# Optimization experiments

Hardware: AMD Instinct MI355X
Metric: run time of the kernel (lower is better)

The kernel has to match this reference:

```python
import jax, jax.numpy as jnp
import numpy as np

T, BS, N = 256, 512, 2048
FUDGE = 1e-4


def setup_inputs() -> dict:
    key = jax.random.key(0)
    ks = jax.random.split(key, 6)
    f32 = jnp.float32
    return {
        "noises": jax.random.normal(ks[0], (T, BS), f32) * 0.1,  # per-step process noise [T, bs]
        "ys": jax.random.normal(ks[1], (T,), f32),               # per-step scalar targets
        "qs": jax.random.normal(ks[2], (T,), f32),               # per-step scalar context input
        "z_biases": jax.random.normal(ks[3], (N,), f32),         # random-feature bias directions
        "w_in": jax.random.normal(ks[4], (N,), f32),             # random input weights
        "w_inq": jax.random.normal(ks[5], (N,), f32),            # random q-input weights
        # scalar learned params (legacy init values)
        "log_learning_rate": jnp.array(-6.0, f32),
        "log_learning_rate_decay": jnp.array(0.0, f32),
        "sigma_b": jnp.array(0.1, f32),
        "output_scale": jnp.array(1.0, f32),
        "u_feedback_scale": jnp.array(1.0, f32),
        "log_weight_decay": jnp.array(-0.001, f32),
        "q_scale": jnp.array(1.0, f32),
        "tauqlpf_m1": jnp.array(-1.0, f32),
        "tauylpf_m1": jnp.array(-1.0, f32),
    }


def _forward(noises, ys, qs, z_biases, w_in, w_inq,
             log_learning_rate, log_learning_rate_decay, sigma_b,
             output_scale, u_feedback_scale, log_weight_decay, q_scale,
             tauqlpf_m1, tauylpf_m1):
    bs = noises.shape[1]
    n = w_in.shape[0]
    softplus = lambda v: jnp.log1p(jnp.exp(v))
    biases = sigma_b * z_biases                    # [n]
    lr0 = jnp.exp(log_learning_rate)               # scalar
    tauq = 1.0 + softplus(tauqlpf_m1)
    tauy = 1.0 + softplus(tauylpf_m1)
    wd = jnp.exp(log_weight_decay)                 # tie_lr_weight_decay=False -> scalar decay
    lr_decay_rate = jnp.exp(log_learning_rate_decay)

    def step(carry, inp):
        w_out, u, e, lr_mult, qlp, ylp = carry
        y, noise_x, q = inp
        qlp = (1.0 - tauq) * qlp + tauq * q
        q_in = w_inq * (q_scale * qlp)             # [n]
        x = u * u_feedback_scale + e + noise_x     # noise injected at node 'x'; [bs]
        h = jax.nn.relu(biases[None, :] + x[:, None] * w_in[None, :] + q_in[None, :])  # [bs, n]
        u = jnp.einsum('kj,kj->k', w_out, h)       # [bs]
        a_mean = output_scale * u                  # [bs]
        # y observed every step (no None/NaN branch)
        ylp = (1.0 - tauy) * ylp + tauy * y
        e = ylp - u                                # [bs]
        lr = lr0 * lr_mult                         # [bs]
        dw = e[:, None] * h * lr[:, None]          # [bs, n]
        w_out = w_out + dw
        norms = jnp.sqrt(FUDGE + jnp.sum(dw * dw, axis=1))
        lr_mult = lr_mult * jnp.exp(-lr_decay_rate * norms)
        w_out = wd * w_out
        return (w_out, u, e, lr_mult, qlp, ylp), a_mean

    init = (jnp.zeros((bs, n), noises.dtype),
            jnp.zeros((bs,), noises.dtype),
            jnp.zeros((bs,), noises.dtype),
            jnp.ones((bs,), noises.dtype),
            jnp.zeros((), noises.dtype),
            jnp.zeros((), noises.dtype))
    _, a_means = jax.lax.scan(step, init, (ys, noises, qs))
    return a_means  # [T, bs]


def reference(noises, ys, qs, z_biases, w_in, w_inq,
              log_learning_rate, log_learning_rate_decay, sigma_b,
              output_scale, u_feedback_scale, log_weight_decay, q_scale,
              tauqlpf_m1, tauylpf_m1):
    return _forward(noises, ys, qs, z_biases, w_in, w_inq,
                    log_learning_rate, log_learning_rate_decay, sigma_b,
                    output_scale, u_feedback_scale, log_weight_decay, q_scale,
                    tauqlpf_m1, tauylpf_m1)
```

## Files before the change

kernel.cpp:

```cpp
#include <hip/hip_runtime.h>
#include <math.h>
#include <stdint.h>

#define T_STEPS 256
#define BS      512
#define N       2048
#define BLOCK   64
#define FUDGE   1e-4f

__global__ __launch_bounds__(BLOCK) __attribute__((amdgpu_waves_per_eu(1, 1)))
void legacy_elbo_scan_kernel(
    const float* __restrict__ noises,
    const float* __restrict__ ys,
    const float* __restrict__ qs,
    const float* __restrict__ z_biases,
    const float* __restrict__ w_in,
    const float* __restrict__ w_inq,
    const float* __restrict__ p_llr,
    const float* __restrict__ p_llrd,
    const float* __restrict__ p_sigb,
    const float* __restrict__ p_oscale,
    const float* __restrict__ p_ufs,
    const float* __restrict__ p_lwd,
    const float* __restrict__ p_qscale,
    const float* __restrict__ p_tauq,
    const float* __restrict__ p_tauy,
    float* __restrict__ out)
{
    const int tid = threadIdx.x;
    const int blk = blockIdx.x;

    const float sigb    = p_sigb[0];
    const float lr0     = expf(p_llr[0]);
    const float lr_decay= expf(p_llrd[0]);
    const float wd      = expf(p_lwd[0]);
    const float rwd     = 1.0f / wd;
    const float tauq    = 1.0f + log1pf(expf(p_tauq[0]));
    const float tauy    = 1.0f + log1pf(expf(p_tauy[0]));
    const float omtq    = 1.0f - tauq;
    const float omty    = 1.0f - tauy;
    const float qscale  = p_qscale[0];
    const float ufs     = p_ufs[0];
    const float oscale  = p_oscale[0];
    const float nld2    = -lr_decay * 1.4426950408889634f;

    const float* nzp = noises + blk;
    const int    ovo = blk * 4;

    asm volatile(
        "v_lshlrev_b32 v7, 4, %[vtid]\n\t"
        "v_add_u32 v5, 0x1000, v7\n\t"
        "global_load_dwordx4 v[32:35],  v7, %[pzb]\n\t"
        "global_load_dwordx4 v[36:39],  v7, %[pzb] offset:1024\n\t"
        "global_load_dwordx4 v[40:43],  v7, %[pzb] offset:2048\n\t"
        "global_load_dwordx4 v[44:47],  v7, %[pzb] offset:3072\n\t"
        "global_load_dwordx4 v[48:51],  v5, %[pzb]\n\t"
        "global_load_dwordx4 v[52:55],  v5, %[pzb] offset:1024\n\t"
        "global_load_dwordx4 v[56:59],  v5, %[pzb] offset:2048\n\t"
        "global_load_dwordx4 v[60:63],  v5, %[pzb] offset:3072\n\t"
        "global_load_dwordx4 v[64:67],  v7, %[pwi]\n\t"
        "global_load_dwordx4 v[68:71],  v7, %[pwi] offset:1024\n\t"
        "global_load_dwordx4 v[72:75],  v7, %[pwi] offset:2048\n\t"
        "global_load_dwordx4 v[76:79],  v7, %[pwi] offset:3072\n\t"
        "global_load_dwordx4 v[80:83],  v5, %[pwi]\n\t"
        "global_load_dwordx4 v[84:87],  v5, %[pwi] offset:1024\n\t"
        "global_load_dwordx4 v[88:91],  v5, %[pwi] offset:2048\n\t"
        "global_load_dwordx4 v[92:95],  v5, %[pwi] offset:3072\n\t"
        "global_load_dwordx4 v[96:99],  v7, %[pwq]\n\t"
        "global_load_dwordx4 v[100:103], v7, %[pwq] offset:1024\n\t"
        "global_load_dwordx4 v[104:107], v7, %[pwq] offset:2048\n\t"
        "global_load_dwordx4 v[108:111], v7, %[pwq] offset:3072\n\t"
        "global_load_dwordx4 v[112:115], v5, %[pwq]\n\t"
        "global_load_dwordx4 v[116:119], v5, %[pwq] offset:1024\n\t"
        "global_load_dwordx4 v[120:123], v5, %[pwq] offset:2048\n\t"
        "global_load_dwordx4 v[124:127], v5, %[pwq] offset:3072\n\t"
        "s_waitcnt vmcnt(0)\n\t"
        "v_mul_f32 v32, %[osg], v32\n\t"  "v_mul_f32 v33, %[osg], v33\n\t"
        "v_mul_f32 v34, %[osg], v34\n\t"  "v_mul_f32 v35, %[osg], v35\n\t"
        "v_mul_f32 v36, %[osg], v36\n\t"  "v_mul_f32 v37, %[osg], v37\n\t"
        "v_mul_f32 v38, %[osg], v38\n\t"  "v_mul_f32 v39, %[osg], v39\n\t"
        "v_mul_f32 v40, %[osg], v40\n\t"  "v_mul_f32 v41, %[osg], v41\n\t"
        "v_mul_f32 v42, %[osg], v42\n\t"  "v_mul_f32 v43, %[osg], v43\n\t"
        "v_mul_f32 v44, %[osg], v44\n\t"  "v_mul_f32 v45, %[osg], v45\n\t"
        "v_mul_f32 v46, %[osg], v46\n\t"  "v_mul_f32 v47, %[osg], v47\n\t"
        "v_mul_f32 v48, %[osg], v48\n\t"  "v_mul_f32 v49, %[osg], v49\n\t"
        "v_mul_f32 v50, %[osg], v50\n\t"  "v_mul_f32 v51, %[osg], v51\n\t"
        "v_mul_f32 v52, %[osg], v52\n\t"  "v_mul_f32 v53, %[osg], v53\n\t"
        "v_mul_f32 v54, %[osg], v54\n\t"  "v_mul_f32 v55, %[osg], v55\n\t"
        "v_mul_f32 v56, %[osg], v56\n\t"  "v_mul_f32 v57, %[osg], v57\n\t"
        "v_mul_f32 v58, %[osg], v58\n\t"  "v_mul_f32 v59, %[osg], v59\n\t"
        "v_mul_f32 v60, %[osg], v60\n\t"  "v_mul_f32 v61, %[osg], v61\n\t"
        "v_mul_f32 v62, %[osg], v62\n\t"  "v_mul_f32 v63, %[osg], v63\n\t"
        "v_mov_b32 v128, 0\n\t" "v_mov_b32 v129, 0\n\t" "v_mov_b32 v130, 0\n\t" "v_mov_b32 v131, 0\n\t"
        "v_mov_b32 v132, 0\n\t" "v_mov_b32 v133, 0\n\t" "v_mov_b32 v134, 0\n\t" "v_mov_b32 v135, 0\n\t"
        "v_mov_b32 v136, 0\n\t" "v_mov_b32 v137, 0\n\t" "v_mov_b32 v138, 0\n\t" "v_mov_b32 v139, 0\n\t"
        "v_mov_b32 v140, 0\n\t" "v_mov_b32 v141, 0\n\t" "v_mov_b32 v142, 0\n\t" "v_mov_b32 v143, 0\n\t"
        "v_mov_b32 v144, 0\n\t" "v_mov_b32 v145, 0\n\t" "v_mov_b32 v146, 0\n\t" "v_mov_b32 v147, 0\n\t"
        "v_mov_b32 v148, 0\n\t" "v_mov_b32 v149, 0\n\t" "v_mov_b32 v150, 0\n\t" "v_mov_b32 v151, 0\n\t"
        "v_mov_b32 v152, 0\n\t" "v_mov_b32 v153, 0\n\t" "v_mov_b32 v154, 0\n\t" "v_mov_b32 v155, 0\n\t"
        "v_mov_b32 v156, 0\n\t" "v_mov_b32 v157, 0\n\t" "v_mov_b32 v158, 0\n\t" "v_mov_b32 v159, 0\n\t"
        "v_mov_b32 v20, 0\n\t" "v_mov_b32 v21, 0\n\t" "v_mov_b32 v22, 0\n\t" "v_mov_b32 v23, 0\n\t"
        "v_mov_b32 v24, 1.0\n\t" "v_mov_b32 v25, 1.0\n\t" "v_mov_b32 v26, 1.0\n\t"
        "v_mov_b32 v6, %[ovo]\n\t"
        "s_mov_b32 s60, 0\n\t"
        "s_mov_b32 s61, 0\n\t"
        "s_mov_b32 s62, 0\n\t"
        "s_load_dword s66, %[pys], s61\n\t"
        "s_load_dword s67, %[pqs], s61\n\t"
        "s_load_dword s68, %[pnz], s62\n\t"
        "s_waitcnt lgkmcnt(0)\n\t"
        "Lelbo0:\n\t"
        "s_add_u32 s63, s61, 4\n\t"
        "s_min_u32 s63, s63, 0x3fc\n\t"
        "s_add_u32 s64, s62, 0x800\n\t"
        "s_min_u32 s64, s64, 0x7f800\n\t"
        "s_load_dword s69, %[pys], s63\n\t"
        "s_load_dword s70, %[pqs], s63\n\t"
        "s_load_dword s71, %[pnz], s64\n\t"
        "v_mov_b32 v30, s67\n\t"
        "v_mul_f32 v20, %[omq], v20\n\t"
        "v_fmac_f32 v20, %[otq], v30\n\t"
        "v_mul_f32 v10, %[oq], v20\n\t"
        "v_mov_b32 v11, v10\n\t"
        "v_mov_b32 v8, s68\n\t"
        "v_add_f32 v8, v23, v8\n\t"
        "v_fmac_f32 v8, %[ouf], v22\n\t"
        "v_mov_b32 v9, v8\n\t"
        "v_mov_b32 v12, 0\n\t" "v_mov_b32 v13, 0\n\t" "v_mov_b32 v14, 0\n\t" "v_mov_b32 v15, 0\n\t"
        "v_mov_b32 v16, 0\n\t" "v_mov_b32 v17, 0\n\t" "v_mov_b32 v18, 0\n\t" "v_mov_b32 v19, 0\n\t"
        "v_pk_fma_f32 v[160:161], v[10:11], v[96:97],  v[32:33]\n\t"
        "v_pk_fma_f32 v[162:163], v[10:11], v[98:99],  v[34:35]\n\t"
        "v_pk_fma_f32 v[164:165], v[10:11], v[100:101], v[36:37]\n\t"
        "v_pk_fma_f32 v[166:167], v[10:11], v[102:103], v[38:39]\n\t"
        "v_pk_fma_f32 v[168:169], v[10:11], v[104:105], v[40:41]\n\t"
        "v_pk_fma_f32 v[170:171], v[10:11], v[106:107], v[42:43]\n\t"
        "v_pk_fma_f32 v[172:173], v[10:11], v[108:109], v[44:45]\n\t"
        "v_pk_fma_f32 v[174:175], v[10:11], v[110:111], v[46:47]\n\t"
        "v_pk_fma_f32 v[176:177], v[10:11], v[112:113], v[48:49]\n\t"
        "v_pk_fma_f32 v[178:179], v[10:11], v[114:115], v[50:51]\n\t"
        "v_pk_fma_f32 v[180:181], v[10:11], v[116:117], v[52:53]\n\t"
        "v_pk_fma_f32 v[182:183], v[10:11], v[118:119], v[54:55]\n\t"
        "v_pk_fma_f32 v[184:185], v[10:11], v[120:121], v[56:57]\n\t"
        "v_pk_fma_f32 v[186:187], v[10:11], v[122:123], v[58:59]\n\t"
        "v_pk_fma_f32 v[188:189], v[10:11], v[124:125], v[60:61]\n\t"
        "v_pk_fma_f32 v[190:191], v[10:11], v[126:127], v[62:63]\n\t"
        "v_pk_fma_f32 v[160:161], v[8:9], v[64:65], v[160:161]\n\t"
        "v_pk_fma_f32 v[162:163], v[8:9], v[66:67], v[162:163]\n\t"
        "v_pk_fma_f32 v[164:165], v[8:9], v[68:69], v[164:165]\n\t"
        "v_pk_fma_f32 v[166:167], v[8:9], v[70:71], v[166:167]\n\t"
        "v_pk_fma_f32 v[168:169], v[8:9], v[72:73], v[168:169]\n\t"
        "v_pk_fma_f32 v[170:171], v[8:9], v[74:75], v[170:171]\n\t"
        "v_pk_fma_f32 v[172:173], v[8:9], v[76:77], v[172:173]\n\t"
        "v_pk_fma_f32 v[174:175], v[8:9], v[78:79], v[174:175]\n\t"
        "v_pk_fma_f32 v[176:177], v[8:9], v[80:81], v[176:177]\n\t"
        "v_pk_fma_f32 v[178:179], v[8:9], v[82:83], v[178:179]\n\t"
        "v_pk_fma_f32 v[180:181], v[8:9], v[84:85], v[180:181]\n\t"
        "v_pk_fma_f32 v[182:183], v[8:9], v[86:87], v[182:183]\n\t"
        "v_pk_fma_f32 v[184:185], v[8:9], v[88:89], v[184:185]\n\t"
        "v_pk_fma_f32 v[186:187], v[8:9], v[90:91], v[186:187]\n\t"
        "v_pk_fma_f32 v[188:189], v[8:9], v[92:93], v[188:189]\n\t"
        "v_pk_fma_f32 v[190:191], v[8:9], v[94:95], v[190:191]\n\t"
        "v_max_f32 v160, 0, v160\n\t" "v_max_f32 v161, 0, v161\n\t"
        "v_max_f32 v162, 0, v162\n\t" "v_max_f32 v163, 0, v163\n\t"
        "v_max_f32 v164, 0, v164\n\t" "v_max_f32 v165, 0, v165\n\t"
        "v_max_f32 v166, 0, v166\n\t" "v_max_f32 v167, 0, v167\n\t"
        "v_max_f32 v168, 0, v168\n\t" "v_max_f32 v169, 0, v169\n\t"
        "v_max_f32 v170, 0, v170\n\t" "v_max_f32 v171, 0, v171\n\t"
        "v_max_f32 v172, 0, v172\n\t" "v_max_f32 v173, 0, v173\n\t"
        "v_max_f32 v174, 0, v174\n\t" "v_max_f32 v175, 0, v175\n\t"
        "v_max_f32 v176, 0, v176\n\t" "v_max_f32 v177, 0, v177\n\t"
        "v_max_f32 v178, 0, v178\n\t" "v_max_f32 v179, 0, v179\n\t"
        "v_max_f32 v180, 0, v180\n\t" "v_max_f32 v181, 0, v181\n\t"
        "v_max_f32 v182, 0, v182\n\t" "v_max_f32 v183, 0, v183\n\t"
        "v_max_f32 v184, 0, v184\n\t" "v_max_f32 v185, 0, v185\n\t"
        "v_max_f32 v186, 0, v186\n\t" "v_max_f32 v187, 0, v187\n\t"
        "v_max_f32 v188, 0, v188\n\t" "v_max_f32 v189, 0, v189\n\t"
        "v_max_f32 v190, 0, v190\n\t" "v_max_f32 v191, 0, v191\n\t"
        "v_pk_fma_f32 v[12:13], v[128:129], v[160:161], v[12:13]\n\t"
        "v_pk_fma_f32 v[16:17], v[160:161], v[160:161], v[16:17]\n\t"
        "v_pk_fma_f32 v[14:15], v[130:131], v[162:163], v[14:15]\n\t"
        "v_pk_fma_f32 v[18:19], v[162:163], v[162:163], v[18:19]\n\t"
        "v_pk_fma_f32 v[12:13], v[132:133], v[164:165], v[12:13]\n\t"
        "v_pk_fma_f32 v[16:17], v[164:165], v[164:165], v[16:17]\n\t"
        "v_pk_fma_f32 v[14:15], v[134:135], v[166:167], v[14:15]\n\t"
        "v_pk_fma_f32 v[18:19], v[166:167], v[166:167], v[18:19]\n\t"
        "v_pk_fma_f32 v[12:13], v[136:137], v[168:169], v[12:13]\n\t"
        "v_pk_fma_f32 v[16:17], v[168:169], v[168:169], v[16:17]\n\t"
        "v_pk_fma_f32 v[14:15], v[138:139], v[170:171], v[14:15]\n\t"
        "v_pk_fma_f32 v[18:19], v[170:171], v[170:171], v[18:19]\n\t"
        "v_pk_fma_f32 v[12:13], v[140:141], v[172:173], v[12:13]\n\t"
        "v_pk_fma_f32 v[16:17], v[172:173], v[172:173], v[16:17]\n\t"
        "v_pk_fma_f32 v[14:15], v[142:143], v[174:175], v[14:15]\n\t"
        "v_pk_fma_f32 v[18:19], v[174:175], v[174:175], v[18:19]\n\t"
        "v_pk_fma_f32 v[12:13], v[144:145], v[176:177], v[12:13]\n\t"
        "v_pk_fma_f32 v[16:17], v[176:177], v[176:177], v[16:17]\n\t"
        "v_pk_fma_f32 v[14:15], v[146:147], v[178:179], v[14:15]\n\t"
        "v_pk_fma_f32 v[18:19], v[178:179], v[178:179], v[18:19]\n\t"
        "v_pk_fma_f32 v[12:13], v[148:149], v[180:181], v[12:13]\n\t"
        "v_pk_fma_f32 v[16:17], v[180:181], v[180:181], v[16:17]\n\t"
        "v_pk_fma_f32 v[14:15], v[150:151], v[182:183], v[14:15]\n\t"
        "v_pk_fma_f32 v[18:19], v[182:183], v[182:183], v[18:19]\n\t"
        "v_pk_fma_f32 v[12:13], v[152:153], v[184:185], v[12:13]\n\t"
        "v_pk_fma_f32 v[16:17], v[184:185], v[184:185], v[16:17]\n\t"
        "v_pk_fma_f32 v[14:15], v[154:155], v[186:187], v[14:15]\n\t"
        "v_pk_fma_f32 v[18:19], v[186:187], v[186:187], v[18:19]\n\t"
        "v_pk_fma_f32 v[12:13], v[156:157], v[188:189], v[12:13]\n\t"
        "v_pk_fma_f32 v[16:17], v[188:189], v[188:189], v[16:17]\n\t"
        "v_pk_fma_f32 v[14:15], v[158:159], v[190:191], v[14:15]\n\t"
        "v_pk_fma_f32 v[18:19], v[190:191], v[190:191], v[18:19]\n\t"
        "v_add_f32 v12, v12, v14\n\t"
        "v_add_f32 v13, v13, v15\n\t"
        "v_add_f32 v16, v16, v18\n\t"
        "v_add_f32 v17, v17, v19\n\t"
        "v_add_f32 v12, v12, v13\n\t"
        "v_add_f32 v16, v16, v17\n\t"
        "s_nop 1\n\t"
        "v_mov_b32_dpp v30, v12 row_shr:1 row_mask:0xf bank_mask:0xf\n\t"
        "v_mov_b32_dpp v31, v16 row_shr:1 row_mask:0xf bank_mask:0xf\n\t"
        "v_add_f32 v12, v12, v30\n\t"
        "v_add_f32 v16, v16, v31\n\t"
        "s_nop 0\n\t"
        "v_mov_b32_dpp v30, v12 row_shr:2 row_mask:0xf bank_mask:0xf\n\t"
        "v_mov_b32_dpp v31, v16 row_shr:2 row_mask:0xf bank_mask:0xf\n\t"
        "v_add_f32 v12, v12, v30\n\t"
        "v_add_f32 v16, v16, v31\n\t"
        "s_nop 0\n\t"
        "v_mov_b32_dpp v30, v12 row_shr:4 row_mask:0xf bank_mask:0xf\n\t"
        "v_mov_b32_dpp v31, v16 row_shr:4 row_mask:0xf bank_mask:0xf\n\t"
        "v_add_f32 v12, v12, v30\n\t"
        "v_add_f32 v16, v16, v31\n\t"
        "s_nop 0\n\t"
        "v_mov_b32_dpp v30, v12 row_shr:8 row_mask:0xf bank_mask:0xf\n\t"
        "v_mov_b32_dpp v31, v16 row_shr:8 row_mask:0xf bank_mask:0xf\n\t"
        "v_add_f32 v12, v12, v30\n\t"
        "v_add_f32 v16, v16, v31\n\t"
        "s_nop 0\n\t"
        "v_mov_b32_dpp v30, v12 row_bcast:15 row_mask:0xf bank_mask:0xf\n\t"
        "v_mov_b32_dpp v31, v16 row_bcast:15 row_mask:0xf bank_mask:0xf\n\t"
        "v_add_f32 v12, v12, v30\n\t"
        "v_add_f32 v16, v16, v31\n\t"
        "s_nop 0\n\t"
        "v_mov_b32_dpp v30, v12 row_bcast:31 row_mask:0xf bank_mask:0xf\n\t"
        "v_mov_b32_dpp v31, v16 row_bcast:31 row_mask:0xf bank_mask:0xf\n\t"
        "v_add_f32 v12, v12, v30\n\t"
        "v_add_f32 v16, v16, v31\n\t"
        "s_nop 1\n\t"
        "v_readlane_b32 s74, v12, 63\n\t"
        "v_readlane_b32 s75, v16, 63\n\t"
        "v_mul_f32 v22, s74, v25\n\t"
        "v_mul_f32 v30, %[oos], v22\n\t"
        "s_mov_b64 s[72:73], exec\n\t"
        "s_mov_b64 exec, 1\n\t"
        "global_store_dword v6, v30, %[pou]\n\t"
        "s_mov_b64 exec, s[72:73]\n\t"
        "v_add_u32 v6, 0x800, v6\n\t"
        "v_mov_b32 v30, s66\n\t"
        "v_mul_f32 v21, %[omy], v21\n\t"
        "v_fmac_f32 v21, %[oty], v30\n\t"
        "v_sub_f32 v23, v21, v22\n\t"
        "v_mul_f32 v27, %[olr], v23\n\t"
        "v_mul_f32 v27, v27, v24\n\t"
        "v_mul_f32 v28, v27, v26\n\t"
        "v_mov_b32 v29, v28\n\t"
        "v_pk_fma_f32 v[128:129], v[28:29], v[160:161], v[128:129]\n\t"
        "v_pk_fma_f32 v[130:131], v[28:29], v[162:163], v[130:131]\n\t"
        "v_pk_fma_f32 v[132:133], v[28:29], v[164:165], v[132:133]\n\t"
        "v_pk_fma_f32 v[134:135], v[28:29], v[166:167], v[134:135]\n\t"
        "v_pk_fma_f32 v[136:137], v[28:29], v[168:169], v[136:137]\n\t"
        "v_pk_fma_f32 v[138:139], v[28:29], v[170:171], v[138:139]\n\t"
        "v_pk_fma_f32 v[140:141], v[28:29], v[172:173], v[140:141]\n\t"
        "v_pk_fma_f32 v[142:143], v[28:29], v[174:175], v[142:143]\n\t"
        "v_pk_fma_f32 v[144:145], v[28:29], v[176:177], v[144:145]\n\t"
        "v_pk_fma_f32 v[146:147], v[28:29], v[178:179], v[146:147]\n\t"
        "v_pk_fma_f32 v[148:149], v[28:29], v[180:181], v[148:149]\n\t"
        "v_pk_fma_f32 v[150:151], v[28:29], v[182:183], v[150:151]\n\t"
        "v_pk_fma_f32 v[152:153], v[28:29], v[184:185], v[152:153]\n\t"
        "v_pk_fma_f32 v[154:155], v[28:29], v[186:187], v[154:155]\n\t"
        "v_pk_fma_f32 v[156:157], v[28:29], v[188:189], v[156:157]\n\t"
        "v_pk_fma_f32 v[158:159], v[28:29], v[190:191], v[158:159]\n\t"
        "v_mul_f32 v30, v27, v27\n\t"
        "v_mul_f32 v30, s75, v30\n\t"
        "v_add_f32 v30, 0x38d1b717, v30\n\t"
        "v_sqrt_f32 v30, v30\n\t"
        "s_nop 1\n\t"
        "v_mul_f32 v30, %[ond], v30\n\t"
        "v_exp_f32 v30, v30\n\t"
        "s_nop 1\n\t"
        "v_mul_f32 v24, v24, v30\n\t"
        "v_mul_f32 v25, %[owd], v25\n\t"
        "v_mul_f32 v26, %[orw], v26\n\t"
        "s_waitcnt lgkmcnt(0)\n\t"
        "s_mov_b32 s66, s69\n\t"
        "s_mov_b32 s67, s70\n\t"
        "s_mov_b32 s68, s71\n\t"
        "s_mov_b32 s61, s63\n\t"
        "s_mov_b32 s62, s64\n\t"
        "s_add_u32 s60, s60, 1\n\t"
        "s_cmp_lt_u32 s60, 0x100\n\t"
        "s_cbranch_scc1 Lelbo0\n\t"
        "s_waitcnt vmcnt(0)\n\t"
        :
        : [pys]"s"(ys), [pqs]"s"(qs), [pnz]"s"(nzp), [pou]"s"(out),
          [pzb]"s"(z_biases), [pwi]"s"(w_in), [pwq]"s"(w_inq),
          [vtid]"v"(tid), [ovo]"v"(ovo),
          [osg]"v"(sigb), [otq]"v"(tauq), [omq]"v"(omtq),
          [oty]"v"(tauy), [omy]"v"(omty), [oq]"v"(qscale),
          [ouf]"v"(ufs), [olr]"v"(lr0), [owd]"v"(wd), [orw]"v"(rwd),
          [oos]"v"(oscale), [ond]"v"(nld2)
        : "memory", "scc",
          "s60","s61","s62","s63","s64","s65","s66","s67","s68","s69",
          "s70","s71","s72","s73","s74","s75",
          "v2","v3","v4","v5","v6","v7","v8","v9","v10","v11",
          "v12","v13","v14","v15","v16","v17","v18","v19","v20","v21",
          "v22","v23","v24","v25","v26","v27","v28","v29","v30","v31",
          "v32","v33","v34","v35","v36","v37","v38","v39","v40","v41",
          "v42","v43","v44","v45","v46","v47","v48","v49","v50","v51",
          "v52","v53","v54","v55","v56","v57","v58","v59","v60","v61",
          "v62","v63","v64","v65","v66","v67","v68","v69","v70","v71",
          "v72","v73","v74","v75","v76","v77","v78","v79","v80","v81",
          "v82","v83","v84","v85","v86","v87","v88","v89","v90","v91",
          "v92","v93","v94","v95","v96","v97","v98","v99","v100","v101",
          "v102","v103","v104","v105","v106","v107","v108","v109","v110","v111",
          "v112","v113","v114","v115","v116","v117","v118","v119","v120","v121",
          "v122","v123","v124","v125","v126","v127","v128","v129","v130","v131",
          "v132","v133","v134","v135","v136","v137","v138","v139","v140","v141",
          "v142","v143","v144","v145","v146","v147","v148","v149","v150","v151",
          "v152","v153","v154","v155","v156","v157","v158","v159","v160","v161",
          "v162","v163","v164","v165","v166","v167","v168","v169","v170","v171",
          "v172","v173","v174","v175","v176","v177","v178","v179","v180","v181",
          "v182","v183","v184","v185","v186","v187","v188","v189","v190","v191"
    );
}

extern "C" void kernel_launch(void* const* d_in, const int* in_sizes, int n_in,
                              void* d_out, int out_size, void* d_ws, size_t ws_size,
                              hipStream_t stream) {
    (void)in_sizes; (void)n_in; (void)d_ws; (void)ws_size; (void)out_size;
    const float* noises   = (const float*)d_in[0];
    const float* ys       = (const float*)d_in[1];
    const float* qs       = (const float*)d_in[2];
    const float* z_biases = (const float*)d_in[3];
    const float* w_in     = (const float*)d_in[4];
    const float* w_inq    = (const float*)d_in[5];
    const float* llr      = (const float*)d_in[6];
    const float* llrd     = (const float*)d_in[7];
    const float* sigb     = (const float*)d_in[8];
    const float* oscale   = (const float*)d_in[9];
    const float* ufs      = (const float*)d_in[10];
    const float* lwd      = (const float*)d_in[11];
    const float* qscale   = (const float*)d_in[12];
    const float* tauq     = (const float*)d_in[13];
    const float* tauy     = (const float*)d_in[14];
    float* out = (float*)d_out;

    hipLaunchKernelGGL(legacy_elbo_scan_kernel, dim3(BS), dim3(BLOCK), 0, stream,
                       noises, ys, qs, z_biases, w_in, w_inq,
                       llr, llrd, sigb, oscale, ufs, lwd, qscale, tauq, tauy,
                       out);
}
```

Baseline: 199.4 us.

## Split feature dimension across four waves with LDS cross-wave reduction

Each block grows from one wave to four, and each thread now owns 8 of the 2048 features instead of 32. Register use drops sharply and a block can occupy all SIMDs of a CU. The per-step dot product and squared-norm sums are first reduced within each wave using DPP. The four wave partials are then combined through a double-buffered LDS slot with a barrier every step. This shortens the serial per-step instruction chain, at the cost of a workgroup barrier and an LDS round trip on each of the 256 dependent steps.

```diff
diff --git a/kernel.cpp b/kernel.cpp
--- a/kernel.cpp
+++ b/kernel.cpp
@@ -5,10 +5,10 @@
 #define T_STEPS 256
 #define BS      512
 #define N       2048
-#define BLOCK   64
+#define BLOCK   256
 #define FUDGE   1e-4f
 
-__global__ __launch_bounds__(BLOCK) __attribute__((amdgpu_waves_per_eu(1, 1)))
+__global__ __launch_bounds__(BLOCK, 2)
 void legacy_elbo_scan_kernel(
     const float* __restrict__ noises,
     const float* __restrict__ ys,
@@ -30,6 +30,10 @@
     const int tid = threadIdx.x;
     const int blk = blockIdx.x;
 
+    __shared__ float red_lds[16];
+    if (tid < 16) red_lds[tid] = 0.0f;
+    __syncthreads();
+
     const float sigb    = p_sigb[0];
     const float lr0     = expf(p_llr[0]);
     const float lr_decay= expf(p_llrd[0]);
@@ -48,57 +52,29 @@
     const int    ovo = blk * 4;
 
     asm volatile(
-        "v_lshlrev_b32 v7, 4, %[vtid]\n\t"
-        "v_add_u32 v5, 0x1000, v7\n\t"
-        "global_load_dwordx4 v[32:35],  v7, %[pzb]\n\t"
-        "global_load_dwordx4 v[36:39],  v7, %[pzb] offset:1024\n\t"
-        "global_load_dwordx4 v[40:43],  v7, %[pzb] offset:2048\n\t"
-        "global_load_dwordx4 v[44:47],  v7, %[pzb] offset:3072\n\t"
-        "global_load_dwordx4 v[48:51],  v5, %[pzb]\n\t"
-        "global_load_dwordx4 v[52:55],  v5, %[pzb] offset:1024\n\t"
-        "global_load_dwordx4 v[56:59],  v5, %[pzb] offset:2048\n\t"
-        "global_load_dwordx4 v[60:63],  v5, %[pzb] offset:3072\n\t"
-        "global_load_dwordx4 v[64:67],  v7, %[pwi]\n\t"
-        "global_load_dwordx4 v[68:71],  v7, %[pwi] offset:1024\n\t"
-        "global_load_dwordx4 v[72:75],  v7, %[pwi] offset:2048\n\t"
-        "global_load_dwordx4 v[76:79],  v7, %[pwi] offset:3072\n\t"
-        "global_load_dwordx4 v[80:83],  v5, %[pwi]\n\t"
-        "global_load_dwordx4 v[84:87],  v5, %[pwi] offset:1024\n\t"
-        "global_load_dwordx4 v[88:91],  v5, %[pwi] offset:2048\n\t"
-        "global_load_dwordx4 v[92:95],  v5, %[pwi] offset:3072\n\t"
-        "global_load_dwordx4 v[96:99],  v7, %[pwq]\n\t"
-        "global_load_dwordx4 v[100:103], v7, %[pwq] offset:1024\n\t"
-        "global_load_dwordx4 v[104:107], v7, %[pwq] offset:2048\n\t"
-        "global_load_dwordx4 v[108:111], v7, %[pwq] offset:3072\n\t"
-        "global_load_dwordx4 v[112:115], v5, %[pwq]\n\t"
-        "global_load_dwordx4 v[116:119], v5, %[pwq] offset:1024\n\t"
-        "global_load_dwordx4 v[120:123], v5, %[pwq] offset:2048\n\t"
-        "global_load_dwordx4 v[124:127], v5, %[pwq] offset:3072\n\t"
+        "v_lshrrev_b32 v3, 6, %[vtid]\n\t"
+        "v_lshlrev_b32 v4, 3, v3\n\t"
+        "v_and_b32 v7, 63, %[vtid]\n\t"
+        "v_cmp_eq_u32 vcc, 63, v7\n\t"
+        "s_mov_b64 s[74:75], vcc\n\t"
+        "v_cmp_eq_u32 vcc, 0, %[vtid]\n\t"
+        "s_mov_b64 s[76:77], vcc\n\t"
+        "v_mov_b32 v5, 0\n\t"
+        "v_lshlrev_b32 v1, 4, %[vtid]\n\t"
+        "v_add_u32 v2, 0x1000, v1\n\t"
+        "global_load_dwordx4 v[40:43], v1, %[pzb]\n\t"
+        "global_load_dwordx4 v[44:47], v2, %[pzb]\n\t"
+        "global_load_dwordx4 v[48:51], v1, %[pwi]\n\t"
+        "global_load_dwordx4 v[52:55], v2, %[pwi]\n\t"
+        "global_load_dwordx4 v[56:59], v1, %[pwq]\n\t"
+        "global_load_dwordx4 v[60:63], v2, %[pwq]\n\t"
         "s_waitcnt vmcnt(0)\n\t"
-        "v_mul_f32 v32, %[osg], v32\n\t"  "v_mul_f32 v33, %[osg], v33\n\t"
-        "v_mul_f32 v34, %[osg], v34\n\t"  "v_mul_f32 v35, %[osg], v35\n\t"
-        "v_mul_f32 v36, %[osg], v36\n\t"  "v_mul_f32 v37, %[osg], v37\n\t"
-        "v_mul_f32 v38, %[osg], v38\n\t"  "v_mul_f32 v39, %[osg], v39\n\t"
         "v_mul_f32 v40, %[osg], v40\n\t"  "v_mul_f32 v41, %[osg], v41\n\t"
         "v_mul_f32 v42, %[osg], v42\n\t"  "v_mul_f32 v43, %[osg], v43\n\t"
         "v_mul_f32 v44, %[osg], v44\n\t"  "v_mul_f32 v45, %[osg], v45\n\t"
         "v_mul_f32 v46, %[osg], v46\n\t"  "v_mul_f32 v47, %[osg], v47\n\t"
-        "v_mul_f32 v48, %[osg], v48\n\t"  "v_mul_f32 v49, %[osg], v49\n\t"
-        "v_mul_f32 v50, %[osg], v50\n\t"  "v_mul_f32 v51, %[osg], v51\n\t"
-        "v_mul_f32 v52, %[osg], v52\n\t"  "v_mul_f32 v53, %[osg], v53\n\t"
-        "v_mul_f32 v54, %[osg], v54\n\t"  "v_mul_f32 v55, %[osg], v55\n\t"
-        "v_mul_f32 v56, %[osg], v56\n\t"  "v_mul_f32 v57, %[osg], v57\n\t"
-        "v_mul_f32 v58, %[osg], v58\n\t"  "v_mul_f32 v59, %[osg], v59\n\t"
-        "v_mul_f32 v60, %[osg], v60\n\t"  "v_mul_f32 v61, %[osg], v61\n\t"
-        "v_mul_f32 v62, %[osg], v62\n\t"  "v_mul_f32 v63, %[osg], v63\n\t"
-        "v_mov_b32 v128, 0\n\t" "v_mov_b32 v129, 0\n\t" "v_mov_b32 v130, 0\n\t" "v_mov_b32 v131, 0\n\t"
-        "v_mov_b32 v132, 0\n\t" "v_mov_b32 v133, 0\n\t" "v_mov_b32 v134, 0\n\t" "v_mov_b32 v135, 0\n\t"
-        "v_mov_b32 v136, 0\n\t" "v_mov_b32 v137, 0\n\t" "v_mov_b32 v138, 0\n\t" "v_mov_b32 v139, 0\n\t"
-        "v_mov_b32 v140, 0\n\t" "v_mov_b32 v141, 0\n\t" "v_mov_b32 v142, 0\n\t" "v_mov_b32 v143, 0\n\t"
-        "v_mov_b32 v144, 0\n\t" "v_mov_b32 v145, 0\n\t" "v_mov_b32 v146, 0\n\t" "v_mov_b32 v147, 0\n\t"
-        "v_mov_b32 v148, 0\n\t" "v_mov_b32 v149, 0\n\t" "v_mov_b32 v150, 0\n\t" "v_mov_b32 v151, 0\n\t"
-        "v_mov_b32 v152, 0\n\t" "v_mov_b32 v153, 0\n\t" "v_mov_b32 v154, 0\n\t" "v_mov_b32 v155, 0\n\t"
-        "v_mov_b32 v156, 0\n\t" "v_mov_b32 v157, 0\n\t" "v_mov_b32 v158, 0\n\t" "v_mov_b32 v159, 0\n\t"
+        "v_mov_b32 v64, 0\n\t" "v_mov_b32 v65, 0\n\t" "v_mov_b32 v66, 0\n\t" "v_mov_b32 v67, 0\n\t"
+        "v_mov_b32 v68, 0\n\t" "v_mov_b32 v69, 0\n\t" "v_mov_b32 v70, 0\n\t" "v_mov_b32 v71, 0\n\t"
         "v_mov_b32 v20, 0\n\t" "v_mov_b32 v21, 0\n\t" "v_mov_b32 v22, 0\n\t" "v_mov_b32 v23, 0\n\t"
         "v_mov_b32 v24, 1.0\n\t" "v_mov_b32 v25, 1.0\n\t" "v_mov_b32 v26, 1.0\n\t"
         "v_mov_b32 v6, %[ovo]\n\t"
@@ -109,7 +85,7 @@
         "s_load_dword s67, %[pqs], s61\n\t"
         "s_load_dword s68, %[pnz], s62\n\t"
         "s_waitcnt lgkmcnt(0)\n\t"
-        "Lelbo0:\n\t"
+        "Lelbo2:\n\t"
         "s_add_u32 s63, s61, 4\n\t"
         "s_min_u32 s63, s63, 0x3fc\n\t"
         "s_add_u32 s64, s62, 0x800\n\t"
@@ -126,131 +102,75 @@
         "v_add_f32 v8, v23, v8\n\t"
         "v_fmac_f32 v8, %[ouf], v22\n\t"
         "v_mov_b32 v9, v8\n\t"
-        "v_mov_b32 v12, 0\n\t" "v_mov_b32 v13, 0\n\t" "v_mov_b32 v14, 0\n\t" "v_mov_b32 v15, 0\n\t"
-        "v_mov_b32 v16, 0\n\t" "v_mov_b32 v17, 0\n\t" "v_mov_b32 v18, 0\n\t" "v_mov_b32 v19, 0\n\t"
-        "v_pk_fma_f32 v[160:161], v[10:11], v[96:97],  v[32:33]\n\t"
-        "v_pk_fma_f32 v[162:163], v[10:11], v[98:99],  v[34:35]\n\t"
-        "v_pk_fma_f32 v[164:165], v[10:11], v[100:101], v[36:37]\n\t"
-        "v_pk_fma_f32 v[166:167], v[10:11], v[102:103], v[38:39]\n\t"
-        "v_pk_fma_f32 v[168:169], v[10:11], v[104:105], v[40:41]\n\t"
-        "v_pk_fma_f32 v[170:171], v[10:11], v[106:107], v[42:43]\n\t"
-        "v_pk_fma_f32 v[172:173], v[10:11], v[108:109], v[44:45]\n\t"
-        "v_pk_fma_f32 v[174:175], v[10:11], v[110:111], v[46:47]\n\t"
-        "v_pk_fma_f32 v[176:177], v[10:11], v[112:113], v[48:49]\n\t"
-        "v_pk_fma_f32 v[178:179], v[10:11], v[114:115], v[50:51]\n\t"
-        "v_pk_fma_f32 v[180:181], v[10:11], v[116:117], v[52:53]\n\t"
-        "v_pk_fma_f32 v[182:183], v[10:11], v[118:119], v[54:55]\n\t"
-        "v_pk_fma_f32 v[184:185], v[10:11], v[120:121], v[56:57]\n\t"
-        "v_pk_fma_f32 v[186:187], v[10:11], v[122:123], v[58:59]\n\t"
-        "v_pk_fma_f32 v[188:189], v[10:11], v[124:125], v[60:61]\n\t"
-        "v_pk_fma_f32 v[190:191], v[10:11], v[126:127], v[62:63]\n\t"
-        "v_pk_fma_f32 v[160:161], v[8:9], v[64:65], v[160:161]\n\t"
-        "v_pk_fma_f32 v[162:163], v[8:9], v[66:67], v[162:163]\n\t"
-        "v_pk_fma_f32 v[164:165], v[8:9], v[68:69], v[164:165]\n\t"
-        "v_pk_fma_f32 v[166:167], v[8:9], v[70:71], v[166:167]\n\t"
-        "v_pk_fma_f32 v[168:169], v[8:9], v[72:73], v[168:169]\n\t"
-        "v_pk_fma_f32 v[170:171], v[8:9], v[74:75], v[170:171]\n\t"
-        "v_pk_fma_f32 v[172:173], v[8:9], v[76:77], v[172:173]\n\t"
-        "v_pk_fma_f32 v[174:175], v[8:9], v[78:79], v[174:175]\n\t"
-        "v_pk_fma_f32 v[176:177], v[8:9], v[80:81], v[176:177]\n\t"
-        "v_pk_fma_f32 v[178:179], v[8:9], v[82:83], v[178:179]\n\t"
-        "v_pk_fma_f32 v[180:181], v[8:9], v[84:85], v[180:181]\n\t"
-        "v_pk_fma_f32 v[182:183], v[8:9], v[86:87], v[182:183]\n\t"
-        "v_pk_fma_f32 v[184:185], v[8:9], v[88:89], v[184:185]\n\t"
-        "v_pk_fma_f32 v[186:187], v[8:9], v[90:91], v[186:187]\n\t"
-        "v_pk_fma_f32 v[188:189], v[8:9], v[92:93], v[188:189]\n\t"
-        "v_pk_fma_f32 v[190:191], v[8:9], v[94:95], v[190:191]\n\t"
-        "v_max_f32 v160, 0, v160\n\t" "v_max_f32 v161, 0, v161\n\t"
-        "v_max_f32 v162, 0, v162\n\t" "v_max_f32 v163, 0, v163\n\t"
-        "v_max_f32 v164, 0, v164\n\t" "v_max_f32 v165, 0, v165\n\t"
-        "v_max_f32 v166, 0, v166\n\t" "v_max_f32 v167, 0, v167\n\t"
-        "v_max_f32 v168, 0, v168\n\t" "v_max_f32 v169, 0, v169\n\t"
-        "v_max_f32 v170, 0, v170\n\t" "v_max_f32 v171, 0, v171\n\t"
-        "v_max_f32 v172, 0, v172\n\t" "v_max_f32 v173, 0, v173\n\t"
-        "v_max_f32 v174, 0, v174\n\t" "v_max_f32 v175, 0, v175\n\t"
-        "v_max_f32 v176, 0, v176\n\t" "v_max_f32 v177, 0, v177\n\t"
-        "v_max_f32 v178, 0, v178\n\t" "v_max_f32 v179, 0, v179\n\t"
-        "v_max_f32 v180, 0, v180\n\t" "v_max_f32 v181, 0, v181\n\t"
-        "v_max_f32 v182, 0, v182\n\t" "v_max_f32 v183, 0, v183\n\t"
-        "v_max_f32 v184, 0, v184\n\t" "v_max_f32 v185, 0, v185\n\t"
-        "v_max_f32 v186, 0, v186\n\t" "v_max_f32 v187, 0, v187\n\t"
-        "v_max_f32 v188, 0, v188\n\t" "v_max_f32 v189, 0, v189\n\t"
-        "v_max_f32 v190, 0, v190\n\t" "v_max_f32 v191, 0, v191\n\t"
-        "v_pk_fma_f32 v[12:13], v[128:129], v[160:161], v[12:13]\n\t"
-        "v_pk_fma_f32 v[16:17], v[160:161], v[160:161], v[16:17]\n\t"
-        "v_pk_fma_f32 v[14:15], v[130:131], v[162:163], v[14:15]\n\t"
-        "v_pk_fma_f32 v[18:19], v[162:163], v[162:163], v[18:19]\n\t"
-        "v_pk_fma_f32 v[12:13], v[132:133], v[164:165], v[12:13]\n\t"
-        "v_pk_fma_f32 v[16:17], v[164:165], v[164:165], v[16:17]\n\t"
-        "v_pk_fma_f32 v[14:15], v[134:135], v[166:167], v[14:15]\n\t"
-        "v_pk_fma_f32 v[18:19], v[166:167], v[166:167], v[18:19]\n\t"
-        "v_pk_fma_f32 v[12:13], v[136:137], v[168:169], v[12:13]\n\t"
-        "v_pk_fma_f32 v[16:17], v[168:169], v[168:169], v[16:17]\n\t"
-        "v_pk_fma_f32 v[14:15], v[138:139], v[170:171], v[14:15]\n\t"
-        "v_pk_fma_f32 v[18:19], v[170:171], v[170:171], v[18:19]\n\t"
-        "v_pk_fma_f32 v[12:13], v[140:141], v[172:173], v[12:13]\n\t"
-        "v_pk_fma_f32 v[16:17], v[172:173], v[172:173], v[16:17]\n\t"
-        "v_pk_fma_f32 v[14:15], v[142:143], v[174:175], v[14:15]\n\t"
-        "v_pk_fma_f32 v[18:19], v[174:175], v[174:175], v[18:19]\n\t"
-        "v_pk_fma_f32 v[12:13], v[144:145], v[176:177], v[12:13]\n\t"
-        "v_pk_fma_f32 v[16:17], v[176:177], v[176:177], v[16:17]\n\t"
-        "v_pk_fma_f32 v[14:15], v[146:147], v[178:179], v[14:15]\n\t"
-        "v_pk_fma_f32 v[18:19], v[178:179], v[178:179], v[18:19]\n\t"
-        "v_pk_fma_f32 v[12:13], v[148:149], v[180:181], v[12:13]\n\t"
-        "v_pk_fma_f32 v[16:17], v[180:181], v[180:181], v[16:17]\n\t"
-        "v_pk_fma_f32 v[14:15], v[150:151], v[182:183], v[14:15]\n\t"
-        "v_pk_fma_f32 v[18:19], v[182:183], v[182:183], v[18:19]\n\t"
-        "v_pk_fma_f32 v[12:13], v[152:153], v[184:185], v[12:13]\n\t"
-        "v_pk_fma_f32 v[16:17], v[184:185], v[184:185], v[16:17]\n\t"
-        "v_pk_fma_f32 v[14:15], v[154:155], v[186:187], v[14:15]\n\t"
-        "v_pk_fma_f32 v[18:19], v[186:187], v[186:187], v[18:19]\n\t"
-        "v_pk_fma_f32 v[12:13], v[156:157], v[188:189], v[12:13]\n\t"
-        "v_pk_fma_f32 v[16:17], v[188:189], v[188:189], v[16:17]\n\t"
-        "v_pk_fma_f32 v[14:15], v[158:159], v[190:191], v[14:15]\n\t"
-        "v_pk_fma_f32 v[18:19], v[190:191], v[190:191], v[18:19]\n\t"
-        "v_add_f32 v12, v12, v14\n\t"
-        "v_add_f32 v13, v13, v15\n\t"
-        "v_add_f32 v16, v16, v18\n\t"
-        "v_add_f32 v17, v17, v19\n\t"
+        "v_mov_b32 v12, 0\n\t" "v_mov_b32 v13, 0\n\t"
+        "v_mov_b32 v14, 0\n\t" "v_mov_b32 v15, 0\n\t"
+        "v_pk_fma_f32 v[72:73], v[10:11], v[56:57], v[40:41]\n\t"
+        "v_pk_fma_f32 v[74:75], v[10:11], v[58:59], v[42:43]\n\t"
+        "v_pk_fma_f32 v[76:77], v[10:11], v[60:61], v[44:45]\n\t"
+        "v_pk_fma_f32 v[78:79], v[10:11], v[62:63], v[46:47]\n\t"
+        "v_pk_fma_f32 v[72:73], v[8:9], v[48:49], v[72:73]\n\t"
+        "v_pk_fma_f32 v[74:75], v[8:9], v[50:51], v[74:75]\n\t"
+        "v_pk_fma_f32 v[76:77], v[8:9], v[52:53], v[76:77]\n\t"
+        "v_pk_fma_f32 v[78:79], v[8:9], v[54:55], v[78:79]\n\t"
+        "v_max_f32 v72, 0, v72\n\t" "v_max_f32 v73, 0, v73\n\t"
+        "v_max_f32 v74, 0, v74\n\t" "v_max_f32 v75, 0, v75\n\t"
+        "v_max_f32 v76, 0, v76\n\t" "v_max_f32 v77, 0, v77\n\t"
+        "v_max_f32 v78, 0, v78\n\t" "v_max_f32 v79, 0, v79\n\t"
+        "v_pk_fma_f32 v[12:13], v[64:65], v[72:73], v[12:13]\n\t"
+        "v_pk_fma_f32 v[14:15], v[72:73], v[72:73], v[14:15]\n\t"
+        "v_pk_fma_f32 v[12:13], v[66:67], v[74:75], v[12:13]\n\t"
+        "v_pk_fma_f32 v[14:15], v[74:75], v[74:75], v[14:15]\n\t"
+        "v_pk_fma_f32 v[12:13], v[68:69], v[76:77], v[12:13]\n\t"
+        "v_pk_fma_f32 v[14:15], v[76:77], v[76:77], v[14:15]\n\t"
+        "v_pk_fma_f32 v[12:13], v[70:71], v[78:79], v[12:13]\n\t"
+        "v_pk_fma_f32 v[14:15], v[78:79], v[78:79], v[14:15]\n\t"
         "v_add_f32 v12, v12, v13\n\t"
-        "v_add_f32 v16, v16, v17\n\t"
+        "v_add_f32 v14, v14, v15\n\t"
         "s_nop 1\n\t"
         "v_mov_b32_dpp v30, v12 row_shr:1 row_mask:0xf bank_mask:0xf\n\t"
-        "v_mov_b32_dpp v31, v16 row_shr:1 row_mask:0xf bank_mask:0xf\n\t"
-        "v_add_f32 v12, v12, v30\n\t"
-        "v_add_f32 v16, v16, v31\n\t"
+        "v_mov_b32_dpp v31, v14 row_shr:1 row_mask:0xf bank_mask:0xf\n\t"
+        "v_add_f32 v12, v12, v30\n\t"
+        "v_add_f32 v14, v14, v31\n\t"
         "s_nop 0\n\t"
         "v_mov_b32_dpp v30, v12 row_shr:2 row_mask:0xf bank_mask:0xf\n\t"
-        "v_mov_b32_dpp v31, v16 row_shr:2 row_mask:0xf bank_mask:0xf\n\t"
-        "v_add_f32 v12, v12, v30\n\t"
-        "v_add_f32 v16, v16, v31\n\t"
+        "v_mov_b32_dpp v31, v14 row_shr:2 row_mask:0xf bank_mask:0xf\n\t"
+        "v_add_f32 v12, v12, v30\n\t"
+        "v_add_f32 v14, v14, v31\n\t"
         "s_nop 0\n\t"
         "v_mov_b32_dpp v30, v12 row_shr:4 row_mask:0xf bank_mask:0xf\n\t"
-        "v_mov_b32_dpp v31, v16 row_shr:4 row_mask:0xf bank_mask:0xf\n\t"
-        "v_add_f32 v12, v12, v30\n\t"
-        "v_add_f32 v16, v16, v31\n\t"
+        "v_mov_b32_dpp v31, v14 row_shr:4 row_mask:0xf bank_mask:0xf\n\t"
+        "v_add_f32 v12, v12, v30\n\t"
+        "v_add_f32 v14, v14, v31\n\t"
         "s_nop 0\n\t"
         "v_mov_b32_dpp v30, v12 row_shr:8 row_mask:0xf bank_mask:0xf\n\t"
-        "v_mov_b32_dpp v31, v16 row_shr:8 row_mask:0xf bank_mask:0xf\n\t"
-        "v_add_f32 v12, v12, v30\n\t"
-        "v_add_f32 v16, v16, v31\n\t"
+        "v_mov_b32_dpp v31, v14 row_shr:8 row_mask:0xf bank_mask:0xf\n\t"
+        "v_add_f32 v12, v12, v30\n\t"
+        "v_add_f32 v14, v14, v31\n\t"
         "s_nop 0\n\t"
         "v_mov_b32_dpp v30, v12 row_bcast:15 row_mask:0xf bank_mask:0xf\n\t"
-        "v_mov_b32_dpp v31, v16 row_bcast:15 row_mask:0xf bank_mask:0xf\n\t"
-        "v_add_f32 v12, v12, v30\n\t"
-        "v_add_f32 v16, v16, v31\n\t"
+        "v_mov_b32_dpp v31, v14 row_bcast:15 row_mask:0xf bank_mask:0xf\n\t"
+        "v_add_f32 v12, v12, v30\n\t"
+        "v_add_f32 v14, v14, v31\n\t"
         "s_nop 0\n\t"
         "v_mov_b32_dpp v30, v12 row_bcast:31 row_mask:0xf bank_mask:0xf\n\t"
-        "v_mov_b32_dpp v31, v16 row_bcast:31 row_mask:0xf bank_mask:0xf\n\t"
-        "v_add_f32 v12, v12, v30\n\t"
-        "v_add_f32 v16, v16, v31\n\t"
-        "s_nop 1\n\t"
-        "v_readlane_b32 s74, v12, 63\n\t"
-        "v_readlane_b32 s75, v16, 63\n\t"
-        "v_mul_f32 v22, s74, v25\n\t"
+        "v_mov_b32_dpp v31, v14 row_bcast:31 row_mask:0xf bank_mask:0xf\n\t"
+        "v_add_f32 v12, v12, v30\n\t"
+        "v_add_f32 v14, v14, v31\n\t"
+        "s_nop 1\n\t"
+        "s_and_saveexec_b64 s[72:73], s[74:75]\n\t"
+        "ds_write2_b32 v4, v12, v14 offset0:0 offset1:1\n\t"
+        "s_mov_b64 exec, s[72:73]\n\t"
+        "s_waitcnt lgkmcnt(0)\n\t"
+        "s_barrier\n\t"
+        "ds_read_b128 v[32:35], v5\n\t"
+        "ds_read_b128 v[36:39], v5 offset:16\n\t"
+        "s_waitcnt lgkmcnt(0)\n\t"
+        "v_pk_add_f32 v[32:33], v[32:33], v[34:35]\n\t"
+        "v_pk_add_f32 v[36:37], v[36:37], v[38:39]\n\t"
+        "v_pk_add_f32 v[32:33], v[32:33], v[36:37]\n\t"
+        "v_mul_f32 v22, v25, v32\n\t"
         "v_mul_f32 v30, %[oos], v22\n\t"
-        "s_mov_b64 s[72:73], exec\n\t"
-        "s_mov_b64 exec, 1\n\t"
+        "s_and_saveexec_b64 s[72:73], s[76:77]\n\t"
         "global_store_dword v6, v30, %[pou]\n\t"
         "s_mov_b64 exec, s[72:73]\n\t"
         "v_add_u32 v6, 0x800, v6\n\t"
@@ -262,24 +182,12 @@
         "v_mul_f32 v27, v27, v24\n\t"
         "v_mul_f32 v28, v27, v26\n\t"
         "v_mov_b32 v29, v28\n\t"
-        "v_pk_fma_f32 v[128:129], v[28:29], v[160:161], v[128:129]\n\t"
-        "v_pk_fma_f32 v[130:131], v[28:29], v[162:163], v[130:131]\n\t"
-        "v_pk_fma_f32 v[132:133], v[28:29], v[164:165], v[132:133]\n\t"
-        "v_pk_fma_f32 v[134:135], v[28:29], v[166:167], v[134:135]\n\t"
-        "v_pk_fma_f32 v[136:137], v[28:29], v[168:169], v[136:137]\n\t"
-        "v_pk_fma_f32 v[138:139], v[28:29], v[170:171], v[138:139]\n\t"
-        "v_pk_fma_f32 v[140:141], v[28:29], v[172:173], v[140:141]\n\t"
-        "v_pk_fma_f32 v[142:143], v[28:29], v[174:175], v[142:143]\n\t"
-        "v_pk_fma_f32 v[144:145], v[28:29], v[176:177], v[144:145]\n\t"
-        "v_pk_fma_f32 v[146:147], v[28:29], v[178:179], v[146:147]\n\t"
-        "v_pk_fma_f32 v[148:149], v[28:29], v[180:181], v[148:149]\n\t"
-        "v_pk_fma_f32 v[150:151], v[28:29], v[182:183], v[150:151]\n\t"
-        "v_pk_fma_f32 v[152:153], v[28:29], v[184:185], v[152:153]\n\t"
-        "v_pk_fma_f32 v[154:155], v[28:29], v[186:187], v[154:155]\n\t"
-        "v_pk_fma_f32 v[156:157], v[28:29], v[188:189], v[156:157]\n\t"
-        "v_pk_fma_f32 v[158:159], v[28:29], v[190:191], v[158:159]\n\t"
+        "v_pk_fma_f32 v[64:65], v[28:29], v[72:73], v[64:65]\n\t"
+        "v_pk_fma_f32 v[66:67], v[28:29], v[74:75], v[66:67]\n\t"
+        "v_pk_fma_f32 v[68:69], v[28:29], v[76:77], v[68:69]\n\t"
+        "v_pk_fma_f32 v[70:71], v[28:29], v[78:79], v[70:71]\n\t"
         "v_mul_f32 v30, v27, v27\n\t"
-        "v_mul_f32 v30, s75, v30\n\t"
+        "v_mul_f32 v30, v33, v30\n\t"
         "v_add_f32 v30, 0x38d1b717, v30\n\t"
         "v_sqrt_f32 v30, v30\n\t"
         "s_nop 1\n\t"
@@ -289,6 +197,8 @@
         "v_mul_f32 v24, v24, v30\n\t"
         "v_mul_f32 v25, %[owd], v25\n\t"
         "v_mul_f32 v26, %[orw], v26\n\t"
+        "v_xor_b32 v4, 32, v4\n\t"
+        "v_xor_b32 v5, 32, v5\n\t"
         "s_waitcnt lgkmcnt(0)\n\t"
         "s_mov_b32 s66, s69\n\t"
         "s_mov_b32 s67, s70\n\t"
@@ -297,7 +207,7 @@
         "s_mov_b32 s62, s64\n\t"
         "s_add_u32 s60, s60, 1\n\t"
         "s_cmp_lt_u32 s60, 0x100\n\t"
-        "s_cbranch_scc1 Lelbo0\n\t"
+        "s_cbranch_scc1 Lelbo2\n\t"
         "s_waitcnt vmcnt(0)\n\t"
         :
         : [pys]"s"(ys), [pqs]"s"(qs), [pnz]"s"(nzp), [pou]"s"(out),
@@ -307,28 +217,17 @@
           [oty]"v"(tauy), [omy]"v"(omty), [oq]"v"(qscale),
           [ouf]"v"(ufs), [olr]"v"(lr0), [owd]"v"(wd), [orw]"v"(rwd),
           [oos]"v"(oscale), [ond]"v"(nld2)
-        : "memory", "scc",
+        : "memory", "scc", "vcc",
           "s60","s61","s62","s63","s64","s65","s66","s67","s68","s69",
-          "s70","s71","s72","s73","s74","s75",
-          "v2","v3","v4","v5","v6","v7","v8","v9","v10","v11",
+          "s70","s71","s72","s73","s74","s75","s76","s77",
+          "v1","v2","v3","v4","v5","v6","v7","v8","v9","v10","v11",
           "v12","v13","v14","v15","v16","v17","v18","v19","v20","v21",
           "v22","v23","v24","v25","v26","v27","v28","v29","v30","v31",
           "v32","v33","v34","v35","v36","v37","v38","v39","v40","v41",
           "v42","v43","v44","v45","v46","v47","v48","v49","v50","v51",
           "v52","v53","v54","v55","v56","v57","v58","v59","v60","v61",
           "v62","v63","v64","v65","v66","v67","v68","v69","v70","v71",
-          "v72","v73","v74","v75","v76","v77","v78","v79","v80","v81",
-          "v82","v83","v84","v85","v86","v87","v88","v89","v90","v91",
-          "v92","v93","v94","v95","v96","v97","v98","v99","v100","v101",
-          "v102","v103","v104","v105","v106","v107","v108","v109","v110","v111",
-          "v112","v113","v114","v115","v116","v117","v118","v119","v120","v121",
-          "v122","v123","v124","v125","v126","v127","v128","v129","v130","v131",
-          "v132","v133","v134","v135","v136","v137","v138","v139","v140","v141",
-          "v142","v143","v144","v145","v146","v147","v148","v149","v150","v151",
-          "v152","v153","v154","v155","v156","v157","v158","v159","v160","v161",
-          "v162","v163","v164","v165","v166","v167","v168","v169","v170","v171",
-          "v172","v173","v174","v175","v176","v177","v178","v179","v180","v181",
-          "v182","v183","v184","v185","v186","v187","v188","v189","v190","v191"
+          "v72","v73","v74","v75","v76","v77","v78","v79"
     );
 }
 
@@ -353,7 +252,7 @@
     const float* tauy     = (const float*)d_in[14];
     float* out = (float*)d_out;
 
-    hipLaunchKernelGGL(legacy_elbo_scan_kernel, dim3(BS), dim3(BLOCK), 0, stream,
+    hipLaunchKernelGGL(legacy_elbo_scan_kernel, dim3(BS), dim3(BLOCK), 64, stream,
                        noises, ys, qs, z_biases, w_in, w_inq,
                        llr, llrd, sigb, oscale, ufs, lwd, qscale, tauq, tauy,
                        out);
```

Result: slower. 203.4 us (+2.0%).
